# Kernel optimization log

Measured on AMD Instinct MI355X. Metric: run time of the kernel, lower is better.

## Reference

```python
import jax, jax.numpy as jnp
import numpy as np

B, N, H, W = 16, 16, 512, 512


def setup_inputs() -> dict:
    key = jax.random.key(0)
    k1, k2, k3, k4, k5, k6 = jax.random.split(key, 6)
    # binary-ish segmentation masks (float, as in torch)
    masks = (jax.random.uniform(k1, (B, N, H, W)) < 0.3).astype(jnp.float32)
    target_mask = (jax.random.uniform(k2, (B, H, W)) < 0.3).astype(jnp.float32)
    # well-formed boxes: x1<x2, y1<y2, all within [0, W)/[0, H)
    x1 = jax.random.randint(k3, (B, N), 0, W // 2)
    y1 = jax.random.randint(k4, (B, N), 0, H // 2)
    wdt = jax.random.randint(k5, (B, N), 1, W // 2)
    hgt = jax.random.randint(k6, (B, N), 1, H // 2)
    boxes = jnp.stack([x1, y1, x1 + wdt, y1 + hgt], axis=-1).astype(jnp.int32)  # (B,N,4) xyxy
    return {"masks": masks, "target_mask": target_mask, "boxes": boxes}


def _edge_features(masks, target_mask, boxes):
    # masks: (B,N,H,W) float; target_mask: (B,H,W) float; boxes: (B,N,4) int xyxy
    # target_overlap[b,n] = sum(masks[b,n] * target_mask[b])  (torch loop body, vectorized)
    overlap = jnp.einsum("bnhw,bhw->bn", masks, target_mask)

    x1, y1, x2, y2 = boxes[..., 0], boxes[..., 1], boxes[..., 2], boxes[..., 3]  # (B,N)
    rows = jnp.arange(H)  # (H,)
    cols = jnp.arange(W)  # (W,)
    # separable box-mask indicators: box_mask[b,n,h,w] = row_in[b,n,h] * col_in[b,n,w]
    row_in = ((rows[None, None, :] >= y1[..., None]) & (rows[None, None, :] < y2[..., None])).astype(masks.dtype)  # (B,N,H)
    col_in = ((cols[None, None, :] >= x1[..., None]) & (cols[None, None, :] < x2[..., None])).astype(masks.dtype)  # (B,N,W)

    # intersection = sum(box_mask * target_mask) without materializing (B,N,H,W)
    intersection = jnp.einsum("bnh,bnw,bhw->bn", row_in, col_in, target_mask)
    box_area = row_in.sum(-1) * col_in.sum(-1)              # (B,N)
    target_area = target_mask.sum((-2, -1))                 # (B,)
    union = box_area + target_area[:, None] - intersection
    iou = intersection / (union + 1e-8)

    return jnp.stack([overlap, iou], axis=-1)  # (B,N,2)


def reference(masks, target_mask, boxes):
    return _edge_features(masks, target_mask, boxes)
```

## Files before the change

### kernel.cpp

```cpp
#include <hip/hip_runtime.h>

constexpr int B = 16, N = 16, H = 512, W = 512;
constexpr int HW = H * W;
constexpr int THREADS = 1024;
constexpr int NWAVE = THREADS / 64;

typedef float floatx4 __attribute__((ext_vector_type(4)));

__global__ __launch_bounds__(THREADS) void fused_kernel(
    const float* __restrict__ masks,
    const float* __restrict__ target,
    const int*   __restrict__ boxes,
    float* __restrict__ out)
{
    const int i0   = blockIdx.x;
    const int xcd  = i0 & 7;
    const int slot = i0 >> 3;
    const int b    = xcd * 2 + (slot >> 4);
    const int n    = slot & 15;
    const int bn   = b * N + n;

    const int x1 = boxes[bn * 4 + 0];
    const int y1 = boxes[bn * 4 + 1];
    const int x2 = boxes[bn * 4 + 2];
    const int y2 = boxes[bn * 4 + 3];

    const floatx4* m4 = (const floatx4*)(masks + (size_t)bn * HW);
    const floatx4* t4 = (const floatx4*)(target + (size_t)b * HW);

    float ov = 0.f, inter = 0.f, ts = 0.f;
    #pragma unroll 8
    for (int i = threadIdx.x; i < HW / 4; i += THREADS) {
        floatx4 m = __builtin_nontemporal_load(&m4[i]);
        floatx4 t = t4[i];
        ov += m.x * t.x + m.y * t.y + m.z * t.z + m.w * t.w;
        ts += t.x + t.y + t.z + t.w;
        int h = i >> 7;
        int w = (i & 127) << 2;
        if (h >= y1 && h < y2) {
            if (w     >= x1 && w     < x2) inter += t.x;
            if (w + 1 >= x1 && w + 1 < x2) inter += t.y;
            if (w + 2 >= x1 && w + 2 < x2) inter += t.z;
            if (w + 3 >= x1 && w + 3 < x2) inter += t.w;
        }
    }

    for (int off = 32; off > 0; off >>= 1) {
        ov    += __shfl_down(ov, off);
        inter += __shfl_down(inter, off);
        ts    += __shfl_down(ts, off);
    }
    __shared__ float red[3][NWAVE];
    const int wave = threadIdx.x >> 6;
    if ((threadIdx.x & 63) == 0) {
        red[0][wave] = ov;
        red[1][wave] = inter;
        red[2][wave] = ts;
    }
    __syncthreads();
    if (threadIdx.x == 0) {
        float o = 0.f, it = 0.f, t = 0.f;
        #pragma unroll
        for (int k = 0; k < NWAVE; ++k) { o += red[0][k]; it += red[1][k]; t += red[2][k]; }
        int bw = min(x2, W) - max(x1, 0); if (bw < 0) bw = 0;
        int bh = min(y2, H) - max(y1, 0); if (bh < 0) bh = 0;
        float box_area = (float)bw * (float)bh;
        float uni = box_area + t - it;
        out[bn * 2 + 0] = o;
        out[bn * 2 + 1] = it / (uni + 1e-8f);
    }
}

extern "C" void kernel_launch(void* const* d_in, const int* in_sizes, int n_in,
                              void* d_out, int out_size, void* d_ws, size_t ws_size,
                              hipStream_t stream) {
    const float* masks  = (const float*)d_in[0];
    const float* target = (const float*)d_in[1];
    const int*   boxes  = (const int*)d_in[2];
    float* out = (float*)d_out;

    fused_kernel<<<B * N, THREADS, 0, stream>>>(masks, target, boxes, out);
}
```

Baseline: 357.6 us.

## Split each (b,n) reduction across two blocks with atomic cross-block combine

Each (b,n) pair is now handled by two 512-thread blocks instead of one 1024-thread block, each covering half the image rows. Partial sums go into a workspace via atomicAdd, and a per-pair counter lets the last-arriving block compute the final outputs. The aim is more, smaller blocks to fill the GPU's CUs better than 256 large blocks do. In exchange it adds a memset launch, global atomics and a threadfence, and mask data is still read once in total.

```diff
diff --git a/kernel.cpp b/kernel.cpp
--- a/kernel.cpp
+++ b/kernel.cpp
@@ -2,8 +2,11 @@
 
 constexpr int B = 16, N = 16, H = 512, W = 512;
 constexpr int HW = H * W;
-constexpr int THREADS = 1024;
-constexpr int NWAVE = THREADS / 64;
+constexpr int S = 2;
+constexpr int CHUNK = HW / S;
+constexpr int THREADS = 512;
+constexpr int NBLK = B * N * S;
+constexpr int BN = B * N;
 
 typedef float floatx4 __attribute__((ext_vector_type(4)));
 
@@ -11,13 +14,15 @@
     const float* __restrict__ masks,
     const float* __restrict__ target,
     const int*   __restrict__ boxes,
+    float* __restrict__ ws,
     float* __restrict__ out)
 {
     const int i0   = blockIdx.x;
     const int xcd  = i0 & 7;
     const int slot = i0 >> 3;
-    const int b    = xcd * 2 + (slot >> 4);
-    const int n    = slot & 15;
+    const int b    = xcd * 2 + (slot >> 5);
+    const int n    = (slot >> 1) & 15;
+    const int s    = slot & 1;
     const int bn   = b * N + n;
 
     const int x1 = boxes[bn * 4 + 0];
@@ -25,17 +30,18 @@
     const int x2 = boxes[bn * 4 + 2];
     const int y2 = boxes[bn * 4 + 3];
 
-    const floatx4* m4 = (const floatx4*)(masks + (size_t)bn * HW);
-    const floatx4* t4 = (const floatx4*)(target + (size_t)b * HW);
+    const floatx4* m4 = (const floatx4*)(masks + (size_t)bn * HW + (size_t)s * CHUNK);
+    const floatx4* t4 = (const floatx4*)(target + (size_t)b * HW + (size_t)s * CHUNK);
+    const int base_h = (s * CHUNK) >> 9;
 
     float ov = 0.f, inter = 0.f, ts = 0.f;
     #pragma unroll 8
-    for (int i = threadIdx.x; i < HW / 4; i += THREADS) {
+    for (int i = threadIdx.x; i < CHUNK / 4; i += THREADS) {
         floatx4 m = __builtin_nontemporal_load(&m4[i]);
         floatx4 t = t4[i];
         ov += m.x * t.x + m.y * t.y + m.z * t.z + m.w * t.w;
         ts += t.x + t.y + t.z + t.w;
-        int h = i >> 7;
+        int h = base_h + (i >> 7);
         int w = (i & 127) << 2;
         if (h >= y1 && h < y2) {
             if (w     >= x1 && w     < x2) inter += t.x;
@@ -50,7 +56,7 @@
         inter += __shfl_down(inter, off);
         ts    += __shfl_down(ts, off);
     }
-    __shared__ float red[3][NWAVE];
+    __shared__ float red[3][THREADS / 64];
     const int wave = threadIdx.x >> 6;
     if ((threadIdx.x & 63) == 0) {
         red[0][wave] = ov;
@@ -58,16 +64,30 @@
         red[2][wave] = ts;
     }
     __syncthreads();
+
     if (threadIdx.x == 0) {
         float o = 0.f, it = 0.f, t = 0.f;
         #pragma unroll
-        for (int k = 0; k < NWAVE; ++k) { o += red[0][k]; it += red[1][k]; t += red[2][k]; }
-        int bw = min(x2, W) - max(x1, 0); if (bw < 0) bw = 0;
-        int bh = min(y2, H) - max(y1, 0); if (bh < 0) bh = 0;
-        float box_area = (float)bw * (float)bh;
-        float uni = box_area + t - it;
-        out[bn * 2 + 0] = o;
-        out[bn * 2 + 1] = it / (uni + 1e-8f);
+        for (int k = 0; k < THREADS / 64; ++k) {
+            o += red[0][k]; it += red[1][k]; t += red[2][k];
+        }
+        atomicAdd(&ws[0 * BN + bn], o);
+        atomicAdd(&ws[1 * BN + bn], it);
+        atomicAdd(&ws[2 * BN + bn], t);
+        __threadfence();
+        int* ctr = (int*)(ws + 3 * BN);
+        int old = atomicAdd(&ctr[bn], 1);
+        if (old == S - 1) {
+            float O  = atomicAdd(&ws[0 * BN + bn], 0.f);
+            float IT = atomicAdd(&ws[1 * BN + bn], 0.f);
+            float T  = atomicAdd(&ws[2 * BN + bn], 0.f);
+            int bw = min(x2, W) - max(x1, 0); if (bw < 0) bw = 0;
+            int bh = min(y2, H) - max(y1, 0); if (bh < 0) bh = 0;
+            float box_area = (float)bw * (float)bh;
+            float uni = box_area + T - IT;
+            out[bn * 2 + 0] = O;
+            out[bn * 2 + 1] = IT / (uni + 1e-8f);
+        }
     }
 }
 
@@ -78,6 +98,8 @@
     const float* target = (const float*)d_in[1];
     const int*   boxes  = (const int*)d_in[2];
     float* out = (float*)d_out;
+    float* ws  = (float*)d_ws;
 
-    fused_kernel<<<B * N, THREADS, 0, stream>>>(masks, target, boxes, out);
+    hipMemsetAsync(ws, 0, 4 * BN * sizeof(float), stream);
+    fused_kernel<<<NBLK, THREADS, 0, stream>>>(masks, target, boxes, ws, out);
 }
```

Result: slower. 386.5 us (+8.1%).
